# Kernel optimization log

Hardware: AMD Instinct MI355X
Metric: run time of the kernel (lower is better)

Reference implementation:

```python
import jax, jax.numpy as jnp
import numpy as np

N_NODES = 50000
N_EDGES = 800000
NEG_SLOPE = 0.2  # PyG GATConv default negative_slope


def setup_inputs() -> dict:
    key = jax.random.key(0)
    ks = jax.random.split(key, 10)
    d_in, hid, heads = 128, 32, 8

    def glorot(k, shape):
        fan_in, fan_out = shape[0], shape[-1]
        s = jnp.sqrt(2.0 / (fan_in + fan_out)).astype(jnp.float32)
        return jax.random.normal(k, shape, jnp.float32) * s

    return {
        "x": jax.random.normal(ks[0], (N_NODES, d_in), jnp.float32),
        "edge_index": jax.random.randint(ks[1], (2, N_EDGES), 0, N_NODES),
        "W1": glorot(ks[2], (d_in, heads * hid)),
        "a1_src": glorot(ks[3], (heads, hid)),
        "a1_dst": glorot(ks[4], (heads, hid)),
        "b1": jnp.zeros((heads * hid,), jnp.float32),
        "W2": glorot(ks[5], (heads * hid, hid)),
        "a2_src": glorot(ks[6], (1, hid)),
        "a2_dst": glorot(ks[7], (1, hid)),
        "b2": jnp.zeros((hid,), jnp.float32),
    }


def _gat_layer(x, src, dst, W, a_src, a_dst, b, concat):
    # PyG GATConv: h = x @ W, split into heads; alpha_e = softmax_over_dst(
    #   leaky_relu(<h[src], a_src> + <h[dst], a_dst>)); out = scatter-sum alpha*h[src].
    N = x.shape[0]
    H, D = a_src.shape
    h = (x @ W).reshape(N, H, D)                      # [N, H, D]
    score_s = jnp.einsum("nhd,hd->nh", h, a_src)      # [N, H]
    score_d = jnp.einsum("nhd,hd->nh", h, a_dst)
    e = jax.nn.leaky_relu(score_s[src] + score_d[dst], NEG_SLOPE)  # [E, H]
    # numerically-stable softmax over incoming edges per destination node
    m = jax.ops.segment_max(e, dst, num_segments=N)
    ex = jnp.exp(e - m[dst])
    denom = jax.ops.segment_sum(ex, dst, num_segments=N)
    alpha = ex / (denom[dst] + 1e-16)                 # [E, H]
    out = jax.ops.segment_sum(alpha[:, :, None] * h[src], dst, num_segments=N)  # [N, H, D]
    out = out.reshape(N, H * D) if concat else out[:, 0]
    return out + b


def reference(x, edge_index, W1, a1_src, a1_dst, b1, W2, a2_src, a2_dst, b2):
    N = x.shape[0]
    # PyG GATConv add_self_loops=True
    loop = jnp.arange(N, dtype=edge_index.dtype)
    src = jnp.concatenate([edge_index[0], loop])
    dst = jnp.concatenate([edge_index[1], loop])
    h = _gat_layer(x, src, dst, W1, a1_src, a1_dst, b1, concat=True)
    h = jax.nn.relu(h)
    # dropout(p=0.4) is identity in eval mode (deterministic reference)
    return _gat_layer(h, src, dst, W2, a2_src, a2_dst, b2, concat=False)
```

## Files before the change

### kernel.cpp

```cpp
#include <hip/hip_runtime.h>
#include <hip/hip_fp16.h>
#include <math.h>

#define N_NODES 50000
#define N_EDGES 800000
#define E_TOT (N_EDGES + N_NODES)
#define N_RT 3125
#define CAP 64

typedef unsigned int uint;
typedef unsigned short ushort;
typedef float f32x4 __attribute__((ext_vector_type(4)));
typedef short v8s __attribute__((ext_vector_type(8)));

__device__ __forceinline__ ushort f2bf(float f) {
    uint u = __float_as_uint(f);
    return (ushort)((u + 0x7FFFu + ((u >> 16) & 1u)) >> 16);
}
__device__ __forceinline__ float bf2f(ushort u) {
    return __uint_as_float((uint)u << 16);
}
__device__ __forceinline__ float bflo(uint v) { return __uint_as_float(v << 16); }
__device__ __forceinline__ float bfhi(uint v) { return __uint_as_float(v & 0xFFFF0000u); }

__device__ __forceinline__ int kmap(int g, int j) {
    return ((j >> 2) << 4) + (g << 2) + (j & 3);
}


__global__ void wprep_k(const float* __restrict__ W1, const float* __restrict__ a1s,
                        const float* __restrict__ a1d, const float* __restrict__ W2,
                        ushort* __restrict__ W1f, ushort* __restrict__ W2b,
                        ushort* __restrict__ W2r, ushort* __restrict__ Abf,
                        ushort* __restrict__ Arf, int* __restrict__ cnt) {
    for (int i = blockIdx.x * 256 + threadIdx.x; i < N_NODES; i += 21 * 256)
        cnt[i] = 0;

    if (blockIdx.x < 16) {
        int idx = blockIdx.x * 256 + threadIdx.x;
        int lane = idx & 63, ks = (idx >> 6) & 3, ct = idx >> 8;
        int g = lane >> 4, col = ct * 16 + (lane & 15);
        ushort us[8];
        #pragma unroll
        for (int j = 0; j < 8; j++) {
            int k = ks * 32 + kmap(g, j);
            us[j] = f2bf(W1[(size_t)k * 256 + col]);
        }
        uint4 pk;
        pk.x = (uint)us[0] | ((uint)us[1] << 16);
        pk.y = (uint)us[2] | ((uint)us[3] << 16);
        pk.z = (uint)us[4] | ((uint)us[5] << 16);
        pk.w = (uint)us[6] | ((uint)us[7] << 16);
        *((uint4*)(W1f + ((size_t)(ct * 4 + ks) * 64 + lane) * 8)) = pk;
    } else if (blockIdx.x < 20) {
        int idx = (blockIdx.x - 16) * 256 + threadIdx.x;
        int lane = idx & 63, ks = (idx >> 6) & 7, ct = idx >> 9;
        int g = lane >> 4, col = ct * 16 + (lane & 15);
        ushort ub[8], ur[8];
        #pragma unroll
        for (int j = 0; j < 8; j++) {
            int k = ks * 32 + kmap(g, j);
            float v = W2[(size_t)k * 32 + col];
            ub[j] = f2bf(v);
            ur[j] = f2bf(v - bf2f(ub[j]));
        }
        uint4 pb, pr;
        pb.x = (uint)ub[0] | ((uint)ub[1] << 16);
        pb.y = (uint)ub[2] | ((uint)ub[3] << 16);
        pb.z = (uint)ub[4] | ((uint)ub[5] << 16);
        pb.w = (uint)ub[6] | ((uint)ub[7] << 16);
        pr.x = (uint)ur[0] | ((uint)ur[1] << 16);
        pr.y = (uint)ur[2] | ((uint)ur[3] << 16);
        pr.z = (uint)ur[4] | ((uint)ur[5] << 16);
        pr.w = (uint)ur[6] | ((uint)ur[7] << 16);
        *((uint4*)(W2b + ((size_t)(ct * 8 + ks) * 64 + lane) * 8)) = pb;
        *((uint4*)(W2r + ((size_t)(ct * 8 + ks) * 64 + lane) * 8)) = pr;
    } else if (blockIdx.x == 20) {
        int t = threadIdx.x;
        int lane = t & 63, ks = t >> 6;
        int jcol = lane & 15, g = lane >> 4;
        int hh = (jcol < 8) ? jcol : jcol - 8;
        const float* a = (jcol < 8) ? (a1s + hh * 32) : (a1d + hh * 32);
        ushort ub[8], ur[8];
        #pragma unroll
        for (int j = 0; j < 8; j++) {
            int k = ks * 32 + kmap(g, j);
            const float* wrow = W1 + (size_t)k * 256 + hh * 32;
            float v = 0.f;
            #pragma unroll 8
            for (int d = 0; d < 32; d++) v = fmaf(wrow[d], a[d], v);
            ub[j] = f2bf(v);
            ur[j] = f2bf(v - bf2f(ub[j]));
        }
        uint4 pb, pr;
        pb.x = (uint)ub[0] | ((uint)ub[1] << 16);
        pb.y = (uint)ub[2] | ((uint)ub[3] << 16);
        pb.z = (uint)ub[4] | ((uint)ub[5] << 16);
        pb.w = (uint)ub[6] | ((uint)ub[7] << 16);
        pr.x = (uint)ur[0] | ((uint)ur[1] << 16);
        pr.y = (uint)ur[2] | ((uint)ur[3] << 16);
        pr.z = (uint)ur[4] | ((uint)ur[5] << 16);
        pr.w = (uint)ur[6] | ((uint)ur[7] << 16);
        *((uint4*)(Abf + ((size_t)ks * 64 + lane) * 8)) = pb;
        *((uint4*)(Arf + ((size_t)ks * 64 + lane) * 8)) = pr;
    }
}


__global__ __launch_bounds__(256) void scat_k(const int* __restrict__ ei,
                                              int* __restrict__ cnt,
                                              ushort* __restrict__ csr) {
    int t = blockIdx.x * 256 + threadIdx.x;
    if (t < N_EDGES / 8) {
        int4 sv0 = ((const int4*)ei)[2 * t];
        int4 sv1 = ((const int4*)ei)[2 * t + 1];
        int4 dv0 = ((const int4*)(ei + N_EDGES))[2 * t];
        int4 dv1 = ((const int4*)(ei + N_EDGES))[2 * t + 1];
        int p0 = atomicAdd(&cnt[dv0.x], 1);
        int p1 = atomicAdd(&cnt[dv0.y], 1);
        int p2 = atomicAdd(&cnt[dv0.z], 1);
        int p3 = atomicAdd(&cnt[dv0.w], 1);
        int p4 = atomicAdd(&cnt[dv1.x], 1);
        int p5 = atomicAdd(&cnt[dv1.y], 1);
        int p6 = atomicAdd(&cnt[dv1.z], 1);
        int p7 = atomicAdd(&cnt[dv1.w], 1);
        if (p0 < CAP) csr[dv0.x * CAP + p0] = (ushort)sv0.x;
        if (p1 < CAP) csr[dv0.y * CAP + p1] = (ushort)sv0.y;
        if (p2 < CAP) csr[dv0.z * CAP + p2] = (ushort)sv0.z;
        if (p3 < CAP) csr[dv0.w * CAP + p3] = (ushort)sv0.w;
        if (p4 < CAP) csr[dv1.x * CAP + p4] = (ushort)sv1.x;
        if (p5 < CAP) csr[dv1.y * CAP + p5] = (ushort)sv1.y;
        if (p6 < CAP) csr[dv1.z * CAP + p6] = (ushort)sv1.z;
        if (p7 < CAP) csr[dv1.w * CAP + p7] = (ushort)sv1.w;
    } else if (t < N_EDGES / 8 + (N_NODES + 3) / 4) {
        int n0 = (t - N_EDGES / 8) * 4;
        int p[4];
        #pragma unroll
        for (int j = 0; j < 4; j++) {
            int n = n0 + j;
            p[j] = (n < N_NODES) ? atomicAdd(&cnt[n], 1) : CAP;
        }
        #pragma unroll
        for (int j = 0; j < 4; j++) {
            int n = n0 + j;
            if (n < N_NODES && p[j] < CAP) csr[n * CAP + p[j]] = (ushort)n;
        }
    }
}


__global__ __launch_bounds__(256) void fgemm1_k(
        const float* __restrict__ x, const ushort* __restrict__ W1f,
        const ushort* __restrict__ Abf, const ushort* __restrict__ Arf,
        ushort* __restrict__ h1u, float* __restrict__ s1s,
        float* __restrict__ s1d) {
    int lane = threadIdx.x & 63, wv = threadIdx.x >> 6;
    int rt = blockIdx.x * 4 + wv;
    if (rt >= N_RT) return;
    int r = lane & 15, g = lane >> 4;
    const float* xrow = x + ((size_t)rt * 16 + r) * 128;

    v8s xb[4], xr[4];
    #pragma unroll
    for (int ks = 0; ks < 4; ks++) {
        float4 fa = *((const float4*)(xrow + ks * 32 + g * 4));
        float4 fb = *((const float4*)(xrow + ks * 32 + 16 + g * 4));
        ushort b0 = f2bf(fa.x), b1 = f2bf(fa.y), b2 = f2bf(fa.z), b3 = f2bf(fa.w);
        ushort b4 = f2bf(fb.x), b5 = f2bf(fb.y), b6 = f2bf(fb.z), b7 = f2bf(fb.w);
        uint4 p;
        p.x = (uint)b0 | ((uint)b1 << 16);
        p.y = (uint)b2 | ((uint)b3 << 16);
        p.z = (uint)b4 | ((uint)b5 << 16);
        p.w = (uint)b6 | ((uint)b7 << 16);
        xb[ks] = *((v8s*)&p);
        ushort r0 = f2bf(fa.x - bf2f(b0)), r1 = f2bf(fa.y - bf2f(b1));
        ushort r2 = f2bf(fa.z - bf2f(b2)), r3 = f2bf(fa.w - bf2f(b3));
        ushort r4 = f2bf(fb.x - bf2f(b4)), r5 = f2bf(fb.y - bf2f(b5));
        ushort r6 = f2bf(fb.z - bf2f(b6)), r7 = f2bf(fb.w - bf2f(b7));
        uint4 q;
        q.x = (uint)r0 | ((uint)r1 << 16);
        q.y = (uint)r2 | ((uint)r3 << 16);
        q.z = (uint)r4 | ((uint)r5 << 16);
        q.w = (uint)r6 | ((uint)r7 << 16);
        xr[ks] = *((v8s*)&q);
    }

    f32x4 sacc = (f32x4){0.f, 0.f, 0.f, 0.f};
    const v8s* abp = (const v8s*)Abf;
    const v8s* arp = (const v8s*)Arf;
    #pragma unroll
    for (int ks = 0; ks < 4; ks++) {
        v8s ab = abp[ks * 64 + lane];
        v8s ar = arp[ks * 64 + lane];
        sacc = __builtin_amdgcn_mfma_f32_16x16x32_bf16(ab, xb[ks], sacc, 0, 0, 0);
        sacc = __builtin_amdgcn_mfma_f32_16x16x32_bf16(ar, xb[ks], sacc, 0, 0, 0);
        sacc = __builtin_amdgcn_mfma_f32_16x16x32_bf16(ab, xr[ks], sacc, 0, 0, 0);
    }
    {
        int row = rt * 16 + r;
        float4 sv;
        sv.x = sacc[0]; sv.y = sacc[1]; sv.z = sacc[2]; sv.w = sacc[3];
        if (g < 2) *((float4*)(s1s + (size_t)row * 8 + g * 4)) = sv;
        else       *((float4*)(s1d + (size_t)row * 8 + (g - 2) * 4)) = sv;
    }

    f32x4 acc[16];
    #pragma unroll
    for (int ct = 0; ct < 16; ct++) acc[ct] = (f32x4){0.f, 0.f, 0.f, 0.f};
    const v8s* bp = (const v8s*)W1f;
    #pragma unroll
    for (int ks = 0; ks < 4; ks++) {
        #pragma unroll
        for (int ct = 0; ct < 16; ct++) {
            v8s wf = bp[(ct * 4 + ks) * 64 + lane];
            acc[ct] = __builtin_amdgcn_mfma_f32_16x16x32_bf16(wf, xb[ks], acc[ct], 0, 0, 0);
        }
    }

    ushort* hrow = h1u + ((size_t)rt * 16 + r) * 256;
    #pragma unroll
    for (int ct = 0; ct < 16; ct++) {
        uint lo = (uint)f2bf(acc[ct][0]) | ((uint)f2bf(acc[ct][1]) << 16);
        uint hi = (uint)f2bf(acc[ct][2]) | ((uint)f2bf(acc[ct][3]) << 16);
        *((uint2*)(hrow + ct * 16 + g * 4)) = make_uint2(lo, hi);
    }
}


__global__ __launch_bounds__(256) void agg1_k(
        const ushort* __restrict__ csr, const int* __restrict__ cnt,
        const ushort* __restrict__ h1u, const float* __restrict__ s1s,
        const float* __restrict__ s1d, const float* __restrict__ b1,
        ushort* __restrict__ hrb) {
    __shared__ float els[4][CAP][8];
    int lane = threadIdx.x & 63;
    int wv = threadIdx.x >> 6;
    int n = blockIdx.x * 4 + wv;
    int beg = n * CAP;
    int deg = min(cnt[n], CAP);
    int end = beg + deg;

    int e8 = lane >> 3, h8 = lane & 7;
    float sd = s1d[n * 8 + h8];
    float m = -3.4e38f, d = 0.f;
    for (int i = beg + e8; i < end; i += 8) {
        int s = csr[i];
        float e = s1s[s * 8 + h8] + sd;
        e = (e >= 0.f) ? e : 0.2f * e;
        els[wv][i - beg][h8] = e;
        float mn = fmaxf(m, e);
        d = d * __expf(m - mn) + __expf(e - mn);
        m = mn;
    }
    #pragma unroll
    for (int mask = 8; mask <= 32; mask <<= 1) {
        float om = __shfl_xor(m, mask);
        float od = __shfl_xor(d, mask);
        float nm = fmaxf(m, om);
        d = d * __expf(m - nm) + od * __expf(om - nm);
        m = nm;
    }
    float inv = 1.f / (d + 1e-16f);
    int hB = lane >> 3;
    float mB = __shfl(m, hB);
    float invB = __shfl(inv, hB);

    const uint2* hv = (const uint2*)h1u;
    const float* ep = &els[wv][0][hB];
    float acc0 = 0.f, acc1 = 0.f, acc2 = 0.f, acc3 = 0.f;
    int j = 0;
    for (; j + 3 < deg; j += 4) {
        uint2 cs = *((const uint2*)(csr + beg + j));
        int s0 = cs.x & 0xFFFF, s1 = cs.x >> 16;
        int s2 = cs.y & 0xFFFF, s3 = cs.y >> 16;
        float p0 = __expf(ep[(j + 0) * 8] - mB);
        float p1 = __expf(ep[(j + 1) * 8] - mB);
        float p2 = __expf(ep[(j + 2) * 8] - mB);
        float p3 = __expf(ep[(j + 3) * 8] - mB);
        uint2 v0 = hv[(size_t)s0 * 64 + lane];
        uint2 v1 = hv[(size_t)s1 * 64 + lane];
        uint2 v2 = hv[(size_t)s2 * 64 + lane];
        uint2 v3 = hv[(size_t)s3 * 64 + lane];
        acc0 = fmaf(p0, bflo(v0.x), acc0);
        acc1 = fmaf(p0, bfhi(v0.x), acc1);
        acc2 = fmaf(p0, bflo(v0.y), acc2);
        acc3 = fmaf(p0, bfhi(v0.y), acc3);
        acc0 = fmaf(p1, bflo(v1.x), acc0);
        acc1 = fmaf(p1, bfhi(v1.x), acc1);
        acc2 = fmaf(p1, bflo(v1.y), acc2);
        acc3 = fmaf(p1, bfhi(v1.y), acc3);
        acc0 = fmaf(p2, bflo(v2.x), acc0);
        acc1 = fmaf(p2, bfhi(v2.x), acc1);
        acc2 = fmaf(p2, bflo(v2.y), acc2);
        acc3 = fmaf(p2, bfhi(v2.y), acc3);
        acc0 = fmaf(p3, bflo(v3.x), acc0);
        acc1 = fmaf(p3, bfhi(v3.x), acc1);
        acc2 = fmaf(p3, bflo(v3.y), acc2);
        acc3 = fmaf(p3, bfhi(v3.y), acc3);
    }
    for (; j < deg; j++) {
        int s0 = csr[beg + j];
        float p0 = __expf(ep[j * 8] - mB);
        uint2 v0 = hv[(size_t)s0 * 64 + lane];
        acc0 = fmaf(p0, bflo(v0.x), acc0);
        acc1 = fmaf(p0, bfhi(v0.x), acc1);
        acc2 = fmaf(p0, bflo(v0.y), acc2);
        acc3 = fmaf(p0, bfhi(v0.y), acc3);
    }
    int c0 = 4 * lane;
    float4 bv = *((const float4*)(b1 + c0));
    float o0 = fmaxf(fmaf(acc0, invB, bv.x), 0.f);
    float o1 = fmaxf(fmaf(acc1, invB, bv.y), 0.f);
    float o2 = fmaxf(fmaf(acc2, invB, bv.z), 0.f);
    float o3 = fmaxf(fmaf(acc3, invB, bv.w), 0.f);
    uint lo = (uint)f2bf(o0) | ((uint)f2bf(o1) << 16);
    uint hi = (uint)f2bf(o2) | ((uint)f2bf(o3) << 16);
    ((uint2*)hrb)[(size_t)n * 64 + lane] = make_uint2(lo, hi);
}


__global__ __launch_bounds__(256) void gemm2m_k(
        const ushort* __restrict__ hrb, const ushort* __restrict__ W2b,
        const ushort* __restrict__ W2r, const float* __restrict__ a2s,
        const float* __restrict__ a2d, ushort* __restrict__ h2u,
        float* __restrict__ s2s, float* __restrict__ s2d) {
    int lane = threadIdx.x & 63, wv = threadIdx.x >> 6;
    int rt = blockIdx.x * 4 + wv;
    if (rt >= N_RT) return;
    int r = lane & 15, g = lane >> 4;
    int row = rt * 16 + r;
    const ushort* arow = hrb + (size_t)row * 256;

    v8s af[8];
    #pragma unroll
    for (int ks = 0; ks < 8; ks++) {
        uint2 u0 = *((const uint2*)(arow + ks * 32 + g * 4));
        uint2 u1 = *((const uint2*)(arow + ks * 32 + 16 + g * 4));
        uint4 p; p.x = u0.x; p.y = u0.y; p.z = u1.x; p.w = u1.y;
        af[ks] = *((v8s*)&p);
    }

    f32x4 acc[2];
    acc[0] = (f32x4){0.f, 0.f, 0.f, 0.f};
    acc[1] = (f32x4){0.f, 0.f, 0.f, 0.f};
    const v8s* wbp = (const v8s*)W2b;
    const v8s* wrp = (const v8s*)W2r;
    #pragma unroll
    for (int ks = 0; ks < 8; ks++) {
        #pragma unroll
        for (int ct = 0; ct < 2; ct++) {
            v8s wb = wbp[(ct * 8 + ks) * 64 + lane];
            v8s wr = wrp[(ct * 8 + ks) * 64 + lane];
            acc[ct] = __builtin_amdgcn_mfma_f32_16x16x32_bf16(wb, af[ks], acc[ct], 0, 0, 0);
            acc[ct] = __builtin_amdgcn_mfma_f32_16x16x32_bf16(wr, af[ks], acc[ct], 0, 0, 0);
        }
    }

    float ps = 0.f, pd = 0.f;
    #pragma unroll
    for (int ct = 0; ct < 2; ct++) {
        #pragma unroll
        for (int q = 0; q < 4; q++) {
            int c = ct * 16 + g * 4 + q;
            ps = fmaf(acc[ct][q], a2s[c], ps);
            pd = fmaf(acc[ct][q], a2d[c], pd);
        }
    }
    ps += __shfl_xor(ps, 16); ps += __shfl_xor(ps, 32);
    pd += __shfl_xor(pd, 16); pd += __shfl_xor(pd, 32);
    if (g == 0) { s2s[row] = ps; s2d[row] = pd; }

    #pragma unroll
    for (int ct = 0; ct < 2; ct++) {
        uint lo = (uint)f2bf(acc[ct][0]) | ((uint)f2bf(acc[ct][1]) << 16);
        uint hi = (uint)f2bf(acc[ct][2]) | ((uint)f2bf(acc[ct][3]) << 16);
        *((uint2*)(h2u + (size_t)row * 32 + ct * 16 + g * 4)) = make_uint2(lo, hi);
    }
}


__global__ __launch_bounds__(256) void agg2_k(
        const ushort* __restrict__ csr, const int* __restrict__ cnt,
        const ushort* __restrict__ h2u, const float* __restrict__ s2s,
        const float* __restrict__ s2d, const float* __restrict__ b2,
        float* __restrict__ out) {
    int lane = threadIdx.x & 63;
    int n = blockIdx.x * 4 + (threadIdx.x >> 6);
    int beg = n * CAP;
    int end = beg + min(cnt[n], CAP);
    float sd = s2d[n];

    float m = -3.4e38f, dd = 0.f;
    for (int i = beg + lane; i < end; i += 64) {
        float e = s2s[csr[i]] + sd;
        e = (e >= 0.f) ? e : 0.2f * e;
        float mn = fmaxf(m, e);
        dd = dd * __expf(m - mn) + __expf(e - mn);
        m = mn;
    }
    #pragma unroll
    for (int mask = 1; mask <= 32; mask <<= 1) {
        float om = __shfl_xor(m, mask);
        float od = __shfl_xor(dd, mask);
        float nm = fmaxf(m, om);
        dd = dd * __expf(m - nm) + od * __expf(om - nm);
        m = nm;
    }
    float inv = 1.f / (dd + 1e-16f);

    int e4 = lane >> 4, cp = lane & 15;
    float acc0 = 0.f, acc1 = 0.f;
    for (int c0 = beg; c0 < end; c0 += 64) {
        int i = c0 + lane;
        int sL = 0; float aL = 0.f;
        if (i < end) {
            sL = csr[i];
            float e = s2s[sL] + sd;
            e = (e >= 0.f) ? e : 0.2f * e;
            aL = __expf(e - m) * inv;
        }
        int nsub = min(64, end - c0);
        for (int el = 0; el < nsub; el += 4) {
            int local = el + e4;
            int se = __shfl(sL, local);
            float ae = __shfl(aL, local);
            uint v = *((const uint*)(h2u + (size_t)se * 32 + cp * 2));
            acc0 = fmaf(ae, bflo(v), acc0);
            acc1 = fmaf(ae, bfhi(v), acc1);
        }
    }
    acc0 += __shfl_xor(acc0, 16); acc0 += __shfl_xor(acc0, 32);
    acc1 += __shfl_xor(acc1, 16); acc1 += __shfl_xor(acc1, 32);
    if (lane < 16) {
        float2 bv = ((const float2*)b2)[cp];
        float2 o; o.x = acc0 + bv.x; o.y = acc1 + bv.y;
        ((float2*)(out + (size_t)n * 32))[cp] = o;
    }
}


extern "C" void kernel_launch(void* const* d_in, const int* in_sizes, int n_in,
                              void* d_out, int out_size, void* d_ws, size_t ws_size,
                              hipStream_t stream) {
    const float* x   = (const float*)d_in[0];
    const int*   ei  = (const int*)d_in[1];
    const float* W1  = (const float*)d_in[2];
    const float* a1s = (const float*)d_in[3];
    const float* a1d = (const float*)d_in[4];
    const float* b1  = (const float*)d_in[5];
    const float* W2  = (const float*)d_in[6];
    const float* a2s = (const float*)d_in[7];
    const float* a2d = (const float*)d_in[8];
    const float* b2  = (const float*)d_in[9];
    float* out = (float*)d_out;

    char* w = (char*)d_ws;
    ushort* h1u   = (ushort*)w; w += (size_t)N_NODES * 256 * 2;
    ushort* hrb   = (ushort*)w; w += (size_t)N_NODES * 256 * 2;
    ushort* W1f   = (ushort*)w; w += (size_t)16 * 4 * 64 * 8 * 2;
    ushort* Abf   = (ushort*)w; w += (size_t)4 * 64 * 8 * 2;
    ushort* Arf   = (ushort*)w; w += (size_t)4 * 64 * 8 * 2;
    ushort* W2b   = (ushort*)w; w += (size_t)2 * 8 * 64 * 8 * 2;
    ushort* W2r   = (ushort*)w; w += (size_t)2 * 8 * 64 * 8 * 2;
    ushort* h2u   = (ushort*)w; w += (size_t)N_NODES * 32 * 2;
    float* s1s    = (float*)w;  w += (size_t)N_NODES * 8 * 4;
    float* s1d    = (float*)w;  w += (size_t)N_NODES * 8 * 4;
    float* s2s    = (float*)w;  w += (size_t)N_NODES * 4;
    float* s2d    = (float*)w;  w += (size_t)N_NODES * 4;
    int* cnt    = (int*)w; w += (size_t)N_NODES * 4;
    ushort* csr = (ushort*)w; w += (size_t)N_NODES * CAP * 2;

    int nscat = (N_EDGES / 8 + (N_NODES + 3) / 4 + 255) / 256;

    wprep_k<<<21, 256, 0, stream>>>(W1, a1s, a1d, W2, W1f, W2b, W2r, Abf, Arf, cnt);
    scat_k<<<nscat, 256, 0, stream>>>(ei, cnt, csr);
    fgemm1_k<<<(N_RT + 3) / 4, 256, 0, stream>>>(x, W1f, Abf, Arf, h1u, s1s, s1d);
    agg1_k<<<N_NODES / 4, 256, 0, stream>>>(csr, cnt, h1u, s1s, s1d, b1, hrb);
    gemm2m_k<<<(N_RT + 3) / 4, 256, 0, stream>>>(hrb, W2b, W2r, a2s, a2d, h2u, s2s, s2d);
    agg2_k<<<N_NODES / 4, 256, 0, stream>>>(csr, cnt, h2u, s2s, s2d, b2, out);
}
```

Measured before the change: 212.8 us.

## Fuse layer-1 aggregation with layer-2 GEMM via shared-memory tile

Merges the layer-1 aggregation kernel and the layer-2 projection GEMM into one kernel. Each block aggregates 16 nodes (4 per wave, looped) into a padded LDS tile, then one wave runs the MFMA GEMM on that tile and writes h2, s2s and s2d. This removes the global round trip of the 50000x256 bf16 intermediate and one kernel launch. In exchange the grid has 4x fewer blocks, each wave processes nodes serially, and only one of four waves does the GEMM while the others sit idle after the barrier.

```diff
diff --git a/kernel.cpp b/kernel.cpp
--- a/kernel.cpp
+++ b/kernel.cpp
@@ -227,154 +227,151 @@
 }
 
 
-__global__ __launch_bounds__(256) void agg1_k(
+__global__ __launch_bounds__(256) void agg1g_k(
         const ushort* __restrict__ csr, const int* __restrict__ cnt,
         const ushort* __restrict__ h1u, const float* __restrict__ s1s,
         const float* __restrict__ s1d, const float* __restrict__ b1,
-        ushort* __restrict__ hrb) {
+        const ushort* __restrict__ W2b, const ushort* __restrict__ W2r,
+        const float* __restrict__ a2s, const float* __restrict__ a2d,
+        ushort* __restrict__ h2u, float* __restrict__ s2s,
+        float* __restrict__ s2d) {
     __shared__ float els[4][CAP][8];
+    __shared__ ushort hrt[16][264];
     int lane = threadIdx.x & 63;
     int wv = threadIdx.x >> 6;
-    int n = blockIdx.x * 4 + wv;
-    int beg = n * CAP;
-    int deg = min(cnt[n], CAP);
-    int end = beg + deg;
-
+    int base = blockIdx.x * 16;
     int e8 = lane >> 3, h8 = lane & 7;
-    float sd = s1d[n * 8 + h8];
-    float m = -3.4e38f, d = 0.f;
-    for (int i = beg + e8; i < end; i += 8) {
-        int s = csr[i];
-        float e = s1s[s * 8 + h8] + sd;
-        e = (e >= 0.f) ? e : 0.2f * e;
-        els[wv][i - beg][h8] = e;
-        float mn = fmaxf(m, e);
-        d = d * __expf(m - mn) + __expf(e - mn);
-        m = mn;
-    }
-    #pragma unroll
-    for (int mask = 8; mask <= 32; mask <<= 1) {
-        float om = __shfl_xor(m, mask);
-        float od = __shfl_xor(d, mask);
-        float nm = fmaxf(m, om);
-        d = d * __expf(m - nm) + od * __expf(om - nm);
-        m = nm;
-    }
-    float inv = 1.f / (d + 1e-16f);
     int hB = lane >> 3;
-    float mB = __shfl(m, hB);
-    float invB = __shfl(inv, hB);
-
-    const uint2* hv = (const uint2*)h1u;
-    const float* ep = &els[wv][0][hB];
-    float acc0 = 0.f, acc1 = 0.f, acc2 = 0.f, acc3 = 0.f;
-    int j = 0;
-    for (; j + 3 < deg; j += 4) {
-        uint2 cs = *((const uint2*)(csr + beg + j));
-        int s0 = cs.x & 0xFFFF, s1 = cs.x >> 16;
-        int s2 = cs.y & 0xFFFF, s3 = cs.y >> 16;
-        float p0 = __expf(ep[(j + 0) * 8] - mB);
-        float p1 = __expf(ep[(j + 1) * 8] - mB);
-        float p2 = __expf(ep[(j + 2) * 8] - mB);
-        float p3 = __expf(ep[(j + 3) * 8] - mB);
-        uint2 v0 = hv[(size_t)s0 * 64 + lane];
-        uint2 v1 = hv[(size_t)s1 * 64 + lane];
-        uint2 v2 = hv[(size_t)s2 * 64 + lane];
-        uint2 v3 = hv[(size_t)s3 * 64 + lane];
-        acc0 = fmaf(p0, bflo(v0.x), acc0);
-        acc1 = fmaf(p0, bfhi(v0.x), acc1);
-        acc2 = fmaf(p0, bflo(v0.y), acc2);
-        acc3 = fmaf(p0, bfhi(v0.y), acc3);
-        acc0 = fmaf(p1, bflo(v1.x), acc0);
-        acc1 = fmaf(p1, bfhi(v1.x), acc1);
-        acc2 = fmaf(p1, bflo(v1.y), acc2);
-        acc3 = fmaf(p1, bfhi(v1.y), acc3);
-        acc0 = fmaf(p2, bflo(v2.x), acc0);
-        acc1 = fmaf(p2, bfhi(v2.x), acc1);
-        acc2 = fmaf(p2, bflo(v2.y), acc2);
-        acc3 = fmaf(p2, bfhi(v2.y), acc3);
-        acc0 = fmaf(p3, bflo(v3.x), acc0);
-        acc1 = fmaf(p3, bfhi(v3.x), acc1);
-        acc2 = fmaf(p3, bflo(v3.y), acc2);
-        acc3 = fmaf(p3, bfhi(v3.y), acc3);
-    }
-    for (; j < deg; j++) {
-        int s0 = csr[beg + j];
-        float p0 = __expf(ep[j * 8] - mB);
-        uint2 v0 = hv[(size_t)s0 * 64 + lane];
-        acc0 = fmaf(p0, bflo(v0.x), acc0);
-        acc1 = fmaf(p0, bfhi(v0.x), acc1);
-        acc2 = fmaf(p0, bflo(v0.y), acc2);
-        acc3 = fmaf(p0, bfhi(v0.y), acc3);
-    }
     int c0 = 4 * lane;
     float4 bv = *((const float4*)(b1 + c0));
-    float o0 = fmaxf(fmaf(acc0, invB, bv.x), 0.f);
-    float o1 = fmaxf(fmaf(acc1, invB, bv.y), 0.f);
-    float o2 = fmaxf(fmaf(acc2, invB, bv.z), 0.f);
-    float o3 = fmaxf(fmaf(acc3, invB, bv.w), 0.f);
-    uint lo = (uint)f2bf(o0) | ((uint)f2bf(o1) << 16);
-    uint hi = (uint)f2bf(o2) | ((uint)f2bf(o3) << 16);
-    ((uint2*)hrb)[(size_t)n * 64 + lane] = make_uint2(lo, hi);
-}
-
-
-__global__ __launch_bounds__(256) void gemm2m_k(
-        const ushort* __restrict__ hrb, const ushort* __restrict__ W2b,
-        const ushort* __restrict__ W2r, const float* __restrict__ a2s,
-        const float* __restrict__ a2d, ushort* __restrict__ h2u,
-        float* __restrict__ s2s, float* __restrict__ s2d) {
-    int lane = threadIdx.x & 63, wv = threadIdx.x >> 6;
-    int rt = blockIdx.x * 4 + wv;
-    if (rt >= N_RT) return;
-    int r = lane & 15, g = lane >> 4;
-    int row = rt * 16 + r;
-    const ushort* arow = hrb + (size_t)row * 256;
-
-    v8s af[8];
-    #pragma unroll
-    for (int ks = 0; ks < 8; ks++) {
-        uint2 u0 = *((const uint2*)(arow + ks * 32 + g * 4));
-        uint2 u1 = *((const uint2*)(arow + ks * 32 + 16 + g * 4));
-        uint4 p; p.x = u0.x; p.y = u0.y; p.z = u1.x; p.w = u1.y;
-        af[ks] = *((v8s*)&p);
-    }
-
-    f32x4 acc[2];
-    acc[0] = (f32x4){0.f, 0.f, 0.f, 0.f};
-    acc[1] = (f32x4){0.f, 0.f, 0.f, 0.f};
-    const v8s* wbp = (const v8s*)W2b;
-    const v8s* wrp = (const v8s*)W2r;
-    #pragma unroll
-    for (int ks = 0; ks < 8; ks++) {
+    const uint2* hv = (const uint2*)h1u;
+
+    for (int q = 0; q < 4; q++) {
+        int row = wv * 4 + q;
+        int n = base + row;
+        int beg = n * CAP;
+        int deg = min(cnt[n], CAP);
+        int end = beg + deg;
+
+        float sd = s1d[n * 8 + h8];
+        float m = -3.4e38f, d = 0.f;
+        for (int i = beg + e8; i < end; i += 8) {
+            int s = csr[i];
+            float e = s1s[s * 8 + h8] + sd;
+            e = (e >= 0.f) ? e : 0.2f * e;
+            els[wv][i - beg][h8] = e;
+            float mn = fmaxf(m, e);
+            d = d * __expf(m - mn) + __expf(e - mn);
+            m = mn;
+        }
+        #pragma unroll
+        for (int mask = 8; mask <= 32; mask <<= 1) {
+            float om = __shfl_xor(m, mask);
+            float od = __shfl_xor(d, mask);
+            float nm = fmaxf(m, om);
+            d = d * __expf(m - nm) + od * __expf(om - nm);
+            m = nm;
+        }
+        float inv = 1.f / (d + 1e-16f);
+        float mB = __shfl(m, hB);
+        float invB = __shfl(inv, hB);
+
+        const float* ep = &els[wv][0][hB];
+        float acc0 = 0.f, acc1 = 0.f, acc2 = 0.f, acc3 = 0.f;
+        int j = 0;
+        for (; j + 3 < deg; j += 4) {
+            uint2 cs = *((const uint2*)(csr + beg + j));
+            int s0 = cs.x & 0xFFFF, s1 = cs.x >> 16;
+            int s2 = cs.y & 0xFFFF, s3 = cs.y >> 16;
+            float p0 = __expf(ep[(j + 0) * 8] - mB);
+            float p1 = __expf(ep[(j + 1) * 8] - mB);
+            float p2 = __expf(ep[(j + 2) * 8] - mB);
+            float p3 = __expf(ep[(j + 3) * 8] - mB);
+            uint2 v0 = hv[(size_t)s0 * 64 + lane];
+            uint2 v1 = hv[(size_t)s1 * 64 + lane];
+            uint2 v2 = hv[(size_t)s2 * 64 + lane];
+            uint2 v3 = hv[(size_t)s3 * 64 + lane];
+            acc0 = fmaf(p0, bflo(v0.x), acc0);
+            acc1 = fmaf(p0, bfhi(v0.x), acc1);
+            acc2 = fmaf(p0, bflo(v0.y), acc2);
+            acc3 = fmaf(p0, bfhi(v0.y), acc3);
+            acc0 = fmaf(p1, bflo(v1.x), acc0);
+            acc1 = fmaf(p1, bfhi(v1.x), acc1);
+            acc2 = fmaf(p1, bflo(v1.y), acc2);
+            acc3 = fmaf(p1, bfhi(v1.y), acc3);
+            acc0 = fmaf(p2, bflo(v2.x), acc0);
+            acc1 = fmaf(p2, bfhi(v2.x), acc1);
+            acc2 = fmaf(p2, bflo(v2.y), acc2);
+            acc3 = fmaf(p2, bfhi(v2.y), acc3);
+            acc0 = fmaf(p3, bflo(v3.x), acc0);
+            acc1 = fmaf(p3, bfhi(v3.x), acc1);
+            acc2 = fmaf(p3, bflo(v3.y), acc2);
+            acc3 = fmaf(p3, bfhi(v3.y), acc3);
+        }
+        for (; j < deg; j++) {
+            int s0 = csr[beg + j];
+            float p0 = __expf(ep[j * 8] - mB);
+            uint2 v0 = hv[(size_t)s0 * 64 + lane];
+            acc0 = fmaf(p0, bflo(v0.x), acc0);
+            acc1 = fmaf(p0, bfhi(v0.x), acc1);
+            acc2 = fmaf(p0, bflo(v0.y), acc2);
+            acc3 = fmaf(p0, bfhi(v0.y), acc3);
+        }
+        float o0 = fmaxf(fmaf(acc0, invB, bv.x), 0.f);
+        float o1 = fmaxf(fmaf(acc1, invB, bv.y), 0.f);
+        float o2 = fmaxf(fmaf(acc2, invB, bv.z), 0.f);
+        float o3 = fmaxf(fmaf(acc3, invB, bv.w), 0.f);
+        uint lo = (uint)f2bf(o0) | ((uint)f2bf(o1) << 16);
+        uint hi = (uint)f2bf(o2) | ((uint)f2bf(o3) << 16);
+        *((uint2*)&hrt[row][c0]) = make_uint2(lo, hi);
+    }
+    __syncthreads();
+
+    if (threadIdx.x < 64) {
+        int r = lane & 15, g = lane >> 4;
+        int row = base + r;
+        v8s af[8];
+        #pragma unroll
+        for (int ks = 0; ks < 8; ks++) {
+            uint2 u0 = *((const uint2*)&hrt[r][ks * 32 + g * 4]);
+            uint2 u1 = *((const uint2*)&hrt[r][ks * 32 + 16 + g * 4]);
+            uint4 p; p.x = u0.x; p.y = u0.y; p.z = u1.x; p.w = u1.y;
+            af[ks] = *((v8s*)&p);
+        }
+        f32x4 acc[2];
+        acc[0] = (f32x4){0.f, 0.f, 0.f, 0.f};
+        acc[1] = (f32x4){0.f, 0.f, 0.f, 0.f};
+        const v8s* wbp = (const v8s*)W2b;
+        const v8s* wrp = (const v8s*)W2r;
+        #pragma unroll
+        for (int ks = 0; ks < 8; ks++) {
+            #pragma unroll
+            for (int ct = 0; ct < 2; ct++) {
+                v8s wb = wbp[(ct * 8 + ks) * 64 + lane];
+                v8s wr = wrp[(ct * 8 + ks) * 64 + lane];
+                acc[ct] = __builtin_amdgcn_mfma_f32_16x16x32_bf16(wb, af[ks], acc[ct], 0, 0, 0);
+                acc[ct] = __builtin_amdgcn_mfma_f32_16x16x32_bf16(wr, af[ks], acc[ct], 0, 0, 0);
+            }
+        }
+        float ps = 0.f, pd = 0.f;
         #pragma unroll
         for (int ct = 0; ct < 2; ct++) {
-            v8s wb = wbp[(ct * 8 + ks) * 64 + lane];
-            v8s wr = wrp[(ct * 8 + ks) * 64 + lane];
-            acc[ct] = __builtin_amdgcn_mfma_f32_16x16x32_bf16(wb, af[ks], acc[ct], 0, 0, 0);
-            acc[ct] = __builtin_amdgcn_mfma_f32_16x16x32_bf16(wr, af[ks], acc[ct], 0, 0, 0);
-        }
-    }
-
-    float ps = 0.f, pd = 0.f;
-    #pragma unroll
-    for (int ct = 0; ct < 2; ct++) {
-        #pragma unroll
-        for (int q = 0; q < 4; q++) {
-            int c = ct * 16 + g * 4 + q;
-            ps = fmaf(acc[ct][q], a2s[c], ps);
-            pd = fmaf(acc[ct][q], a2d[c], pd);
-        }
-    }
-    ps += __shfl_xor(ps, 16); ps += __shfl_xor(ps, 32);
-    pd += __shfl_xor(pd, 16); pd += __shfl_xor(pd, 32);
-    if (g == 0) { s2s[row] = ps; s2d[row] = pd; }
-
-    #pragma unroll
-    for (int ct = 0; ct < 2; ct++) {
-        uint lo = (uint)f2bf(acc[ct][0]) | ((uint)f2bf(acc[ct][1]) << 16);
-        uint hi = (uint)f2bf(acc[ct][2]) | ((uint)f2bf(acc[ct][3]) << 16);
-        *((uint2*)(h2u + (size_t)row * 32 + ct * 16 + g * 4)) = make_uint2(lo, hi);
+            #pragma unroll
+            for (int qq = 0; qq < 4; qq++) {
+                int c = ct * 16 + g * 4 + qq;
+                ps = fmaf(acc[ct][qq], a2s[c], ps);
+                pd = fmaf(acc[ct][qq], a2d[c], pd);
+            }
+        }
+        ps += __shfl_xor(ps, 16); ps += __shfl_xor(ps, 32);
+        pd += __shfl_xor(pd, 16); pd += __shfl_xor(pd, 32);
+        if (g == 0) { s2s[row] = ps; s2d[row] = pd; }
+        #pragma unroll
+        for (int ct = 0; ct < 2; ct++) {
+            uint lo = (uint)f2bf(acc[ct][0]) | ((uint)f2bf(acc[ct][1]) << 16);
+            uint hi = (uint)f2bf(acc[ct][2]) | ((uint)f2bf(acc[ct][3]) << 16);
+            *((uint2*)(h2u + (size_t)row * 32 + ct * 16 + g * 4)) = make_uint2(lo, hi);
+        }
     }
 }
 
@@ -456,7 +453,6 @@
 
     char* w = (char*)d_ws;
     ushort* h1u   = (ushort*)w; w += (size_t)N_NODES * 256 * 2;
-    ushort* hrb   = (ushort*)w; w += (size_t)N_NODES * 256 * 2;
     ushort* W1f   = (ushort*)w; w += (size_t)16 * 4 * 64 * 8 * 2;
     ushort* Abf   = (ushort*)w; w += (size_t)4 * 64 * 8 * 2;
     ushort* Arf   = (ushort*)w; w += (size_t)4 * 64 * 8 * 2;
@@ -475,7 +471,7 @@
     wprep_k<<<21, 256, 0, stream>>>(W1, a1s, a1d, W2, W1f, W2b, W2r, Abf, Arf, cnt);
     scat_k<<<nscat, 256, 0, stream>>>(ei, cnt, csr);
     fgemm1_k<<<(N_RT + 3) / 4, 256, 0, stream>>>(x, W1f, Abf, Arf, h1u, s1s, s1d);
-    agg1_k<<<N_NODES / 4, 256, 0, stream>>>(csr, cnt, h1u, s1s, s1d, b1, hrb);
-    gemm2m_k<<<(N_RT + 3) / 4, 256, 0, stream>>>(hrb, W2b, W2r, a2s, a2d, h2u, s2s, s2d);
+    agg1g_k<<<N_NODES / 16, 256, 0, stream>>>(csr, cnt, h1u, s1s, s1d, b1,
+                                              W2b, W2r, a2s, a2d, h2u, s2s, s2d);
     agg2_k<<<N_NODES / 4, 256, 0, stream>>>(csr, cnt, h2u, s2s, s2d, b2, out);
 }
```

Result: faster. 205.8 us (-3.3%).
